# Kernel optimization log

Measured on AMD Instinct MI355X. Metric: run time of the kernel, lower is better.

Reference implementation:

```python
import jax, jax.numpy as jnp
import numpy as np

SEQ_LEN, BATCH, INPUT_SIZE, HIDDEN_SIZE = 2048, 256, 256, 512


def setup_inputs() -> dict:
    key = jax.random.key(0)
    ks = jax.random.split(key, 7)
    s = 1.0 / np.sqrt(HIDDEN_SIZE)  # PyTorch LSTMCell init scale
    inputs = jax.random.normal(ks[0], (SEQ_LEN, BATCH, INPUT_SIZE), dtype=jnp.float32)
    h0 = jnp.zeros((BATCH, HIDDEN_SIZE), dtype=jnp.float32)
    c0 = jnp.zeros((BATCH, HIDDEN_SIZE), dtype=jnp.float32)
    W_ih = jax.random.uniform(ks[1], (4 * HIDDEN_SIZE, INPUT_SIZE), minval=-s, maxval=s, dtype=jnp.float32)
    W_hh = jax.random.uniform(ks[2], (4 * HIDDEN_SIZE, HIDDEN_SIZE), minval=-s, maxval=s, dtype=jnp.float32)
    b_ih = jax.random.uniform(ks[3], (4 * HIDDEN_SIZE,), minval=-s, maxval=s, dtype=jnp.float32)
    b_hh = jax.random.uniform(ks[4], (4 * HIDDEN_SIZE,), minval=-s, maxval=s, dtype=jnp.float32)
    W_dec = jax.random.uniform(ks[5], (1, HIDDEN_SIZE), minval=-s, maxval=s, dtype=jnp.float32)
    b_dec = jax.random.uniform(ks[6], (1,), minval=-s, maxval=s, dtype=jnp.float32)
    return {"inputs": inputs, "h0": h0, "c0": c0, "W_ih": W_ih, "W_hh": W_hh,
            "b_ih": b_ih, "b_hh": b_hh, "W_dec": W_dec, "b_dec": b_dec}


def reference(inputs, h0, c0, W_ih, W_hh, b_ih, b_hh, W_dec, b_dec):
    H = h0.shape[-1]
    # Precompute the input-to-gates projection for all timesteps in one GEMM.
    x_gates = jnp.einsum('tbi,gi->tbg', inputs, W_ih) + b_ih + b_hh  # [T, B, 4H]

    def step(carry, xg):
        h, c = carry
        gates = xg + h @ W_hh.T  # [B, 4H]
        i, f, g, o = jnp.split(gates, 4, axis=-1)  # PyTorch gate order: i, f, g, o
        i = jax.nn.sigmoid(i)
        f = jax.nn.sigmoid(f)
        g = jnp.tanh(g)
        o = jax.nn.sigmoid(o)
        c_new = f * c + i * g
        h_new = o * jnp.tanh(c_new)
        return (h_new, c_new), None

    (h_last, _), _ = jax.lax.scan(step, (h0, c0), x_gates)
    return h_last @ W_dec.T + b_dec  # [B, 1]
```

## Files before the change

kernel.cpp:

```cpp
#include <hip/hip_runtime.h>
#include <math.h>


#define T_STEPS 2048
#define BATCH   256
#define ISZ     256
#define HSZ     512

#define B_GRP 64
#define NGRP  4
#define KSL   8

__device__ __forceinline__ float sigm(float x) { return 1.0f / (1.0f + expf(-x)); }

__global__ __launch_bounds__(512)
void lstm_step_kernel(const float* __restrict__ x_t,
                      const float* __restrict__ W_ih,
                      const float* __restrict__ W_hh,
                      const float* __restrict__ b_ih,
                      const float* __restrict__ b_hh,
                      const float* __restrict__ h_prev,
                      float* __restrict__ h_next,
                      float* __restrict__ c_st)
{
    __shared__ float x_lds[B_GRP][260];

    const int wg  = blockIdx.x;
    const int g   = wg >> 6;
    const int w   = wg & 63;
    const int k0  = w * KSL;
    const int tid = threadIdx.x;

    {
        const int l  = tid & 63;
        const int rb = tid >> 6;
        #pragma unroll
        for (int s = 0; s < 8; ++s) {
            const int row = s * 8 + rb;
            const float4 v = *(const float4*)(x_t + (size_t)(g * B_GRP + row) * ISZ + l * 4);
            *(float4*)(&x_lds[row][l * 4]) = v;
        }
    }
    __syncthreads();

    const int b_l = tid & 63;
    const int b   = g * B_GRP + b_l;
    const int kl  = __builtin_amdgcn_readfirstlane(tid >> 6);
    const int k   = k0 + kl;

    float acc[4];
    #pragma unroll
    for (int q = 0; q < 4; ++q)
        acc[q] = b_ih[q * HSZ + k] + b_hh[q * HSZ + k];

    #pragma unroll 4
    for (int j4 = 0; j4 < ISZ; j4 += 4) {
        const float4 xv = *(const float4*)(&x_lds[b_l][j4]);
        #pragma unroll
        for (int q = 0; q < 4; ++q) {
            const float4 wv = *(const float4*)(W_ih + (size_t)(q * HSZ + k) * ISZ + j4);
            acc[q] += xv.x * wv.x + xv.y * wv.y + xv.z * wv.z + xv.w * wv.w;
        }
    }

    #pragma unroll 4
    for (int j4 = 0; j4 < HSZ; j4 += 4) {
        const float4 hv = *(const float4*)(h_prev + (size_t)(j4 >> 2) * (BATCH * 4) + b * 4);
        #pragma unroll
        for (int q = 0; q < 4; ++q) {
            const float4 wv = *(const float4*)(W_hh + (size_t)(q * HSZ + k) * HSZ + j4);
            acc[q] += hv.x * wv.x + hv.y * wv.y + hv.z * wv.z + hv.w * wv.w;
        }
    }

    const float ig = sigm(acc[0]);
    const float fg = sigm(acc[1]);
    const float gg = tanhf(acc[2]);
    const float og = sigm(acc[3]);

    const int cidx = k * BATCH + b;
    const float c_new = fg * c_st[cidx] + ig * gg;
    c_st[cidx] = c_new;
    h_next[(size_t)(k >> 2) * (BATCH * 4) + b * 4 + (k & 3)] = og * tanhf(c_new);
}

__global__ __launch_bounds__(256)
void lstm_init_kernel(const float* __restrict__ h0, const float* __restrict__ c0,
                      float* __restrict__ hP, float* __restrict__ cT)
{
    const int idx = blockIdx.x * 256 + threadIdx.x;
    const int b = idx >> 9;
    const int k = idx & 511;
    hP[(size_t)(k >> 2) * (BATCH * 4) + b * 4 + (k & 3)] = h0[idx];
    cT[k * BATCH + b] = c0[idx];
}

__global__ __launch_bounds__(256)
void lstm_decode_kernel(const float* __restrict__ hP, const float* __restrict__ W_dec,
                        const float* __restrict__ b_dec, float* __restrict__ out)
{
    const int b = threadIdx.x;
    float s = 0.0f;
    for (int j4 = 0; j4 < HSZ; j4 += 4) {
        const float4 hv = *(const float4*)(hP + (size_t)(j4 >> 2) * (BATCH * 4) + b * 4);
        s += hv.x * W_dec[j4 + 0] + hv.y * W_dec[j4 + 1]
           + hv.z * W_dec[j4 + 2] + hv.w * W_dec[j4 + 3];
    }
    out[b] = s + b_dec[0];
}

extern "C" void kernel_launch(void* const* d_in, const int* in_sizes, int n_in,
                              void* d_out, int out_size, void* d_ws, size_t ws_size,
                              hipStream_t stream) {
    const float* inputs = (const float*)d_in[0];
    const float* h0     = (const float*)d_in[1];
    const float* c0     = (const float*)d_in[2];
    const float* W_ih   = (const float*)d_in[3];
    const float* W_hh   = (const float*)d_in[4];
    const float* b_ih   = (const float*)d_in[5];
    const float* b_hh   = (const float*)d_in[6];
    const float* W_dec  = (const float*)d_in[7];
    const float* b_dec  = (const float*)d_in[8];
    float* out = (float*)d_out;

    float* ws  = (float*)d_ws;
    float* hP0 = ws;
    float* hP1 = ws + 131072;
    float* cT  = ws + 262144;

    hipLaunchKernelGGL(lstm_init_kernel, dim3(512), dim3(256), 0, stream,
                       h0, c0, hP0, cT);

    for (int t = 0; t < T_STEPS; ++t) {
        const float* x_t = inputs + (size_t)t * BATCH * ISZ;
        const float* hp  = (t & 1) ? hP1 : hP0;
        float*       hn  = (t & 1) ? hP0 : hP1;
        hipLaunchKernelGGL(lstm_step_kernel, dim3(NGRP * 64), dim3(512), 0, stream,
                           x_t, W_ih, W_hh, b_ih, b_hh, hp, hn, cT);
    }

    hipLaunchKernelGGL(lstm_decode_kernel, dim3(1), dim3(256), 0, stream,
                       hP0, W_dec, b_dec, out);
}
```

Before: 61.18 ms.

## Split step reduction across two wave groups with LDS combine and swizzled x tile

```diff
diff --git a/kernel.cpp b/kernel.cpp
--- a/kernel.cpp
+++ b/kernel.cpp
@@ -8,12 +8,11 @@
 #define HSZ     512
 
 #define B_GRP 64
-#define NGRP  4
 #define KSL   8
 
 __device__ __forceinline__ float sigm(float x) { return 1.0f / (1.0f + expf(-x)); }
 
-__global__ __launch_bounds__(512)
+__global__ __launch_bounds__(1024)
 void lstm_step_kernel(const float* __restrict__ x_t,
                       const float* __restrict__ W_ih,
                       const float* __restrict__ W_hh,
@@ -23,65 +22,93 @@
                       float* __restrict__ h_next,
                       float* __restrict__ c_st)
 {
-    __shared__ float x_lds[B_GRP][260];
+    __shared__ float4 x_lds[B_GRP * 64];
+    __shared__ float4 red[KSL * B_GRP];
 
-    const int wg  = blockIdx.x;
-    const int g   = wg >> 6;
-    const int w   = wg & 63;
-    const int k0  = w * KSL;
+    const int bid = blockIdx.x;
+    const int rg  = (bid & 7) + ((bid >> 5) << 3);
+    const int g   = (bid >> 3) & 3;
+    const int k0  = rg * KSL;
+
     const int tid = threadIdx.x;
+    const int b_l = tid & 63;
+    const int wid = __builtin_amdgcn_readfirstlane(tid >> 6);
+    const int kl  = wid & 7;
+    const int jh  = wid >> 3;
+    const int k   = k0 + kl;
+    const int b   = g * B_GRP + b_l;
 
-    {
-        const int l  = tid & 63;
-        const int rb = tid >> 6;
-        #pragma unroll
-        for (int s = 0; s < 8; ++s) {
-            const int row = s * 8 + rb;
-            const float4 v = *(const float4*)(x_t + (size_t)(g * B_GRP + row) * ISZ + l * 4);
-            *(float4*)(&x_lds[row][l * 4]) = v;
-        }
+    #pragma unroll
+    for (int s = 0; s < 4; ++s) {
+        const int idx = tid + 1024 * s;
+        const int row = idx >> 6;
+        const int l4  = idx & 63;
+        const float4 v = *(const float4*)(x_t + ((size_t)(g * B_GRP + row) << 8) + (l4 << 2));
+        x_lds[(row << 6) | (l4 ^ (row & 7))] = v;
     }
     __syncthreads();
 
-    const int b_l = tid & 63;
-    const int b   = g * B_GRP + b_l;
-    const int kl  = __builtin_amdgcn_readfirstlane(tid >> 6);
-    const int k   = k0 + kl;
+    float acc0 = 0.f, acc1 = 0.f, acc2 = 0.f, acc3 = 0.f;
 
-    float acc[4];
-    #pragma unroll
-    for (int q = 0; q < 4; ++q)
-        acc[q] = b_ih[q * HSZ + k] + b_hh[q * HSZ + k];
+    if (jh == 0) {
+        #pragma unroll 2
+        for (int j4 = 0; j4 < 64; ++j4) {
+            const float4 xv = x_lds[(b_l << 6) | (j4 ^ (b_l & 7))];
+            const float4 w0 = *(const float4*)(W_ih + (size_t)(0 * HSZ + k) * ISZ + (j4 << 2));
+            const float4 w1 = *(const float4*)(W_ih + (size_t)(1 * HSZ + k) * ISZ + (j4 << 2));
+            const float4 w2 = *(const float4*)(W_ih + (size_t)(2 * HSZ + k) * ISZ + (j4 << 2));
+            const float4 w3 = *(const float4*)(W_ih + (size_t)(3 * HSZ + k) * ISZ + (j4 << 2));
+            acc0 += xv.x * w0.x + xv.y * w0.y + xv.z * w0.z + xv.w * w0.w;
+            acc1 += xv.x * w1.x + xv.y * w1.y + xv.z * w1.z + xv.w * w1.w;
+            acc2 += xv.x * w2.x + xv.y * w2.y + xv.z * w2.z + xv.w * w2.w;
+            acc3 += xv.x * w3.x + xv.y * w3.y + xv.z * w3.z + xv.w * w3.w;
+        }
+        #pragma unroll 2
+        for (int j4 = 0; j4 < 32; ++j4) {
+            const float4 hv = *(const float4*)(h_prev + ((size_t)j4 << 10) + (b << 2));
+            const float4 w0 = *(const float4*)(W_hh + (size_t)(0 * HSZ + k) * HSZ + (j4 << 2));
+            const float4 w1 = *(const float4*)(W_hh + (size_t)(1 * HSZ + k) * HSZ + (j4 << 2));
+            const float4 w2 = *(const float4*)(W_hh + (size_t)(2 * HSZ + k) * HSZ + (j4 << 2));
+            const float4 w3 = *(const float4*)(W_hh + (size_t)(3 * HSZ + k) * HSZ + (j4 << 2));
+            acc0 += hv.x * w0.x + hv.y * w0.y + hv.z * w0.z + hv.w * w0.w;
+            acc1 += hv.x * w1.x + hv.y * w1.y + hv.z * w1.z + hv.w * w1.w;
+            acc2 += hv.x * w2.x + hv.y * w2.y + hv.z * w2.z + hv.w * w2.w;
+            acc3 += hv.x * w3.x + hv.y * w3.y + hv.z * w3.z + hv.w * w3.w;
+        }
+    } else {
+        #pragma unroll 2
+        for (int j4 = 32; j4 < 128; ++j4) {
+            const float4 hv = *(const float4*)(h_prev + ((size_t)j4 << 10) + (b << 2));
+            const float4 w0 = *(const float4*)(W_hh + (size_t)(0 * HSZ + k) * HSZ + (j4 << 2));
+            const float4 w1 = *(const float4*)(W_hh + (size_t)(1 * HSZ + k) * HSZ + (j4 << 2));
+            const float4 w2 = *(const float4*)(W_hh + (size_t)(2 * HSZ + k) * HSZ + (j4 << 2));
+            const float4 w3 = *(const float4*)(W_hh + (size_t)(3 * HSZ + k) * HSZ + (j4 << 2));
+            acc0 += hv.x * w0.x + hv.y * w0.y + hv.z * w0.z + hv.w * w0.w;
+            acc1 += hv.x * w1.x + hv.y * w1.y + hv.z * w1.z + hv.w * w1.w;
+            acc2 += hv.x * w2.x + hv.y * w2.y + hv.z * w2.z + hv.w * w2.w;
+            acc3 += hv.x * w3.x + hv.y * w3.y + hv.z * w3.z + hv.w * w3.w;
+        }
+        red[(kl << 6) | b_l] = make_float4(acc0, acc1, acc2, acc3);
+    }
+    __syncthreads();
 
-    #pragma unroll 4
-    for (int j4 = 0; j4 < ISZ; j4 += 4) {
-        const float4 xv = *(const float4*)(&x_lds[b_l][j4]);
-        #pragma unroll
-        for (int q = 0; q < 4; ++q) {
-            const float4 wv = *(const float4*)(W_ih + (size_t)(q * HSZ + k) * ISZ + j4);
-            acc[q] += xv.x * wv.x + xv.y * wv.y + xv.z * wv.z + xv.w * wv.w;
-        }
+    if (jh == 0) {
+        const float4 r = red[(kl << 6) | b_l];
+        acc0 += r.x + b_ih[0 * HSZ + k] + b_hh[0 * HSZ + k];
+        acc1 += r.y + b_ih[1 * HSZ + k] + b_hh[1 * HSZ + k];
+        acc2 += r.z + b_ih[2 * HSZ + k] + b_hh[2 * HSZ + k];
+        acc3 += r.w + b_ih[3 * HSZ + k] + b_hh[3 * HSZ + k];
+
+        const float ig = sigm(acc0);
+        const float fg = sigm(acc1);
+        const float gg = tanhf(acc2);
+        const float og = sigm(acc3);
+
+        const int cidx = k * BATCH + b;
+        const float c_new = fg * c_st[cidx] + ig * gg;
+        c_st[cidx] = c_new;
+        h_next[((size_t)(k >> 2) << 10) + (b << 2) + (k & 3)] = og * tanhf(c_new);
     }
-
-    #pragma unroll 4
-    for (int j4 = 0; j4 < HSZ; j4 += 4) {
-        const float4 hv = *(const float4*)(h_prev + (size_t)(j4 >> 2) * (BATCH * 4) + b * 4);
-        #pragma unroll
-        for (int q = 0; q < 4; ++q) {
-            const float4 wv = *(const float4*)(W_hh + (size_t)(q * HSZ + k) * HSZ + j4);
-            acc[q] += hv.x * wv.x + hv.y * wv.y + hv.z * wv.z + hv.w * wv.w;
-        }
-    }
-
-    const float ig = sigm(acc[0]);
-    const float fg = sigm(acc[1]);
-    const float gg = tanhf(acc[2]);
-    const float og = sigm(acc[3]);
-
-    const int cidx = k * BATCH + b;
-    const float c_new = fg * c_st[cidx] + ig * gg;
-    c_st[cidx] = c_new;
-    h_next[(size_t)(k >> 2) * (BATCH * 4) + b * 4 + (k & 3)] = og * tanhf(c_new);
 }
 
 __global__ __launch_bounds__(256)
@@ -91,7 +118,7 @@
     const int idx = blockIdx.x * 256 + threadIdx.x;
     const int b = idx >> 9;
     const int k = idx & 511;
-    hP[(size_t)(k >> 2) * (BATCH * 4) + b * 4 + (k & 3)] = h0[idx];
+    hP[((size_t)(k >> 2) << 10) + (b << 2) + (k & 3)] = h0[idx];
     cT[k * BATCH + b] = c0[idx];
 }
 
@@ -102,7 +129,7 @@
     const int b = threadIdx.x;
     float s = 0.0f;
     for (int j4 = 0; j4 < HSZ; j4 += 4) {
-        const float4 hv = *(const float4*)(hP + (size_t)(j4 >> 2) * (BATCH * 4) + b * 4);
+        const float4 hv = *(const float4*)(hP + ((size_t)(j4 >> 2) << 10) + (b << 2));
         s += hv.x * W_dec[j4 + 0] + hv.y * W_dec[j4 + 1]
            + hv.z * W_dec[j4 + 2] + hv.w * W_dec[j4 + 3];
     }
@@ -135,7 +162,7 @@
         const float* x_t = inputs + (size_t)t * BATCH * ISZ;
         const float* hp  = (t & 1) ? hP1 : hP0;
         float*       hn  = (t & 1) ? hP0 : hP1;
-        hipLaunchKernelGGL(lstm_step_kernel, dim3(NGRP * 64), dim3(512), 0, stream,
+        hipLaunchKernelGGL(lstm_step_kernel, dim3(256), dim3(1024), 0, stream,
                            x_t, W_ih, W_hh, b_ih, b_hh, hp, hn, cT);
     }
 
```

Result: faster. 51.85 ms (-15.3%).
